# Kernel tuning notes

Hardware: AMD Instinct MI355X
Metric: run time of the kernel (lower is better)

## Reference

```python
import jax, jax.numpy as jnp
import numpy as np

B, SQ, C = 8, 4096, 1280
CAD = 2048
H, D = 20, 64          # heads x head_dim = hidden_size
NT = 4                 # num IP tokens
TXT = 77               # text tokens
IP_SCALE = 1.0


def setup_inputs() -> dict:
    key = jax.random.key(0)
    ks = jax.random.split(key, 9)
    s = 0.02
    return {
        "hidden_states": jax.random.normal(ks[0], (B, SQ, C), jnp.float32),
        "encoder_hidden_states": jax.random.normal(ks[1], (B, TXT + NT, CAD), jnp.float32),
        "Wq": jax.random.normal(ks[2], (C, C), jnp.float32) * s,
        "Wk": jax.random.normal(ks[3], (CAD, C), jnp.float32) * s,
        "Wv": jax.random.normal(ks[4], (CAD, C), jnp.float32) * s,
        "Wk_ip": jax.random.normal(ks[5], (CAD, C), jnp.float32) * s,
        "Wv_ip": jax.random.normal(ks[6], (CAD, C), jnp.float32) * s,
        "Wo": jax.random.normal(ks[7], (C, C), jnp.float32) * s,
        "bo": jnp.zeros((C,), jnp.float32),
    }


def _heads(x):
    # [b, s, C] -> [b, H, s, D]
    b, s, _ = x.shape
    return x.reshape(b, s, H, D).transpose(0, 2, 1, 3)


def _attend(q, k, v):
    scale = jnp.asarray(1.0 / np.sqrt(D), q.dtype)
    probs = jax.nn.softmax(jnp.einsum('bhqd,bhkd->bhqk', q, k) * scale, axis=-1)
    return jnp.einsum('bhqk,bhkd->bhqd', probs, v)


def reference(hidden_states, encoder_hidden_states, Wq, Wk, Wv, Wk_ip, Wv_ip, Wo, bo):
    residual = hidden_states
    txt = encoder_hidden_states[:, :-NT, :]   # [B, 77, CAD]
    ip = encoder_hidden_states[:, -NT:, :]    # [B, 4, CAD]

    q = _heads(hidden_states @ Wq)            # [B, H, SQ, D]
    k = _heads(txt @ Wk)
    v = _heads(txt @ Wv)
    out = _attend(q, k, v)                    # text branch

    ip_k = _heads(ip @ Wk_ip)
    ip_v = _heads(ip @ Wv_ip)
    out = out + IP_SCALE * _attend(q, ip_k, ip_v)  # IP-adapter branch

    b = out.shape[0]
    out = out.transpose(0, 2, 1, 3).reshape(b, SQ, C)  # merge heads
    out = out @ Wo + bo
    return out + residual
```

## Files before the change

kernel.cpp:

```cpp
#include <hip/hip_runtime.h>
#include <hip/hip_bf16.h>
#include <cstdint>
#include <cstddef>


typedef __bf16 bf16_t;
typedef __bf16 bf16x8 __attribute__((ext_vector_type(8)));
typedef __bf16 bf16x4 __attribute__((ext_vector_type(4)));
typedef float  f32x4  __attribute__((ext_vector_type(4)));
typedef unsigned int u32x4 __attribute__((ext_vector_type(4)));

using as3_void  = __attribute__((address_space(3))) void;
using as1_cvoid = const __attribute__((address_space(1))) void;

#define TXT_ 77

__device__ __forceinline__ bf16x8 ld16(const void* p) {
  u32x4 v = *(const u32x4*)p;
  return __builtin_bit_cast(bf16x8, v);
}

template <int EPI>
__global__ __launch_bounds__(512, 2)
void gemm256(const bf16_t* __restrict__ A, const bf16_t* __restrict__ Bt,
             void* __restrict__ Cout, int ntn, int N, int K,
             const float* __restrict__ bias, const void* __restrict__ residual)
{
  __shared__ __align__(16) char smem[131072];
  const int tid = threadIdx.x, lane = tid & 63, wid = tid >> 6;
  const int wm = wid >> 2, wn = wid & 3;

  const int nwg = gridDim.x;
  int g = blockIdx.x;
  if ((nwg & 7) == 0) g = (blockIdx.x & 7) * (nwg >> 3) + (blockIdx.x >> 3);
  const long bm = (long)(g / ntn) * 256;
  const long bn = (long)(g % ntn) * 256;

  const int NTk = K >> 5;

  const int srow = lane >> 2;
  const int scol = ((lane & 3) ^ ((lane >> 3) & 3)) * 8;

  auto stageA = [&](int t) {
    const int buf = t & 3;
    const long k0 = (long)t << 5;
#pragma unroll
    for (int j = 0; j < 2; ++j) {
      const int ci = j * 8 + wid;
      const bf16_t* gp = A + (bm + ci * 16 + srow) * (long)K + k0 + scol;
      __builtin_amdgcn_global_load_lds((as1_cvoid*)gp,
          (as3_void*)(smem + buf * 16384 + ci * 1024), 16, 0, 0);
    }
  };
  auto stageB = [&](int t) {
    const int buf = t & 3;
    const long k0 = (long)t << 5;
#pragma unroll
    for (int j = 0; j < 2; ++j) {
      const int ci = j * 8 + wid;
      const bf16_t* gp = Bt + (bn + ci * 16 + srow) * (long)K + k0 + scol;
      __builtin_amdgcn_global_load_lds((as1_cvoid*)gp,
          (as3_void*)(smem + 65536 + buf * 16384 + ci * 1024), 16, 0, 0);
    }
  };

  const int l15 = lane & 15, kq = lane >> 4;
  const int rc16 = (kq ^ ((l15 >> 1) & 3)) << 4;

  f32x4 acc[8][4] = {};

  stageA(0); stageB(0); stageA(1); stageB(1);
  asm volatile("s_waitcnt vmcnt(4)" ::: "memory");
  __builtin_amdgcn_s_barrier();

  for (int t = 0; t < NTk; ++t) {
    const char* sa = smem + (t & 3) * 16384;
    const char* sb = smem + 65536 + (t & 3) * 16384;
    bf16x8 bfr[4], afr[4];
#pragma unroll
    for (int n = 0; n < 4; ++n)
      bfr[n] = ld16(sb + (wn * 64 + n * 16 + l15) * 64 + rc16);
#pragma unroll
    for (int m = 0; m < 4; ++m)
      afr[m] = ld16(sa + (wm * 128 + m * 16 + l15) * 64 + rc16);
    if (t + 2 < NTk) stageA(t + 2);
    __builtin_amdgcn_s_setprio(1);
#pragma unroll
    for (int m = 0; m < 4; ++m)
#pragma unroll
      for (int n = 0; n < 4; ++n)
        acc[m][n] = __builtin_amdgcn_mfma_f32_16x16x32_bf16(afr[m], bfr[n], acc[m][n], 0, 0, 0);
    __builtin_amdgcn_s_setprio(0);
#pragma unroll
    for (int m = 0; m < 4; ++m)
      afr[m] = ld16(sa + (wm * 128 + (m + 4) * 16 + l15) * 64 + rc16);
    if (t + 2 < NTk) stageB(t + 2);
    __builtin_amdgcn_s_setprio(1);
#pragma unroll
    for (int m = 0; m < 4; ++m)
#pragma unroll
      for (int n = 0; n < 4; ++n)
        acc[m + 4][n] = __builtin_amdgcn_mfma_f32_16x16x32_bf16(afr[m], bfr[n], acc[m + 4][n], 0, 0, 0);
    __builtin_amdgcn_s_setprio(0);
    if (t == NTk - 2) asm volatile("s_waitcnt vmcnt(0)" ::: "memory");
    else              asm volatile("s_waitcnt vmcnt(4)" ::: "memory");
    __builtin_amdgcn_s_barrier();
    asm volatile("" ::: "memory");
  }

  const int orow0 = (lane >> 4) << 2;
#pragma unroll
  for (int m = 0; m < 8; ++m) {
#pragma unroll
    for (int n = 0; n < 4; ++n) {
      const long col = bn + wn * 64 + n * 16 + l15;
#pragma unroll
      for (int r = 0; r < 4; ++r) {
        const long row = bm + wm * 128 + m * 16 + orow0 + r;
        if constexpr (EPI == 0) {
          ((bf16_t*)Cout)[row * N + col] = (bf16_t)acc[m][n][r];
        } else {
          ((float*)Cout)[row * N + col] =
              acc[m][n][r] + bias[col] +
              (float)((const bf16_t*)residual)[row * N + col];
        }
      }
    }
  }
}

__global__ __launch_bounds__(256, 4)
void gemm_bt(const bf16_t* __restrict__ A, const bf16_t* __restrict__ Bt,
             bf16_t* __restrict__ Cout, int ntn, int N, int K)
{
  __shared__ __align__(16) char smem[2][16384];
  const int tid  = threadIdx.x;
  const int lane = tid & 63;
  const int wid  = tid >> 6;
  const int wm = wid >> 1, wn = wid & 1;

  const int g = blockIdx.x;
  const long bm = (long)(g / ntn) * 128;
  const long bn = (long)(g % ntn) * 128;

  f32x4 acc[4][4] = {};

  const int srow = lane >> 2;
  const int skb  = (lane & 3) ^ (((lane >> 2) ^ (lane >> 4)) & 3);
  const int NT = K >> 5;

  auto stage = [&](int buf, int kt) {
    const int k0 = kt << 5;
#pragma unroll
    for (int cc = 0; cc < 2; ++cc) {
      const int c = wid + cc * 4;
      const bf16_t* ga = A + (bm + c * 16 + srow) * (long)K + (k0 + skb * 8);
      __builtin_amdgcn_global_load_lds((as1_cvoid*)ga,
                                       (as3_void*)(&smem[buf][c * 1024]), 16, 0, 0);
      const bf16_t* gb = Bt + (bn + c * 16 + srow) * (long)K + (k0 + skb * 8);
      __builtin_amdgcn_global_load_lds((as1_cvoid*)gb,
                                       (as3_void*)(&smem[buf][8192 + c * 1024]), 16, 0, 0);
    }
  };

  const int rkb    = (((lane >> 4) ^ (lane & 3) ^ ((lane >> 2) & 3)) & 3) << 4;
  const int rrow_a = wm * 64 + (lane & 15);
  const int rrow_b = wn * 64 + (lane & 15);

  stage(0, 0);
  int cur = 0;
  for (int t = 0; t < NT; ++t) {
    __syncthreads();
    if (t + 1 < NT) stage(cur ^ 1, t + 1);
    const char* sa = smem[cur];
    const char* sb = smem[cur] + 8192;
    bf16x8 af[4], bfv[4];
#pragma unroll
    for (int m = 0; m < 4; ++m)
      af[m] = ld16(sa + (rrow_a + m * 16) * 64 + rkb);
#pragma unroll
    for (int n = 0; n < 4; ++n)
      bfv[n] = ld16(sb + (rrow_b + n * 16) * 64 + rkb);
#pragma unroll
    for (int m = 0; m < 4; ++m)
#pragma unroll
      for (int n = 0; n < 4; ++n)
        acc[m][n] = __builtin_amdgcn_mfma_f32_16x16x32_bf16(af[m], bfv[n], acc[m][n], 0, 0, 0);
    cur ^= 1;
  }

  const int orow0 = wm * 64 + ((lane >> 4) << 2);
  const int ocol0 = wn * 64 + (lane & 15);
#pragma unroll
  for (int m = 0; m < 4; ++m)
#pragma unroll
    for (int n = 0; n < 4; ++n) {
      const long col = bn + ocol0 + n * 16;
#pragma unroll
      for (int r = 0; r < 4; ++r)
        Cout[(bm + orow0 + m * 16 + r) * (long)N + col] = (bf16_t)acc[m][n][r];
    }
}

__global__ __launch_bounds__(256, 3)
void attn_fused(const bf16_t* __restrict__ q, const bf16_t* __restrict__ kvt,
                const bf16_t* __restrict__ kvip, bf16_t* __restrict__ outp)
{
  __shared__ __align__(16) bf16_t K_lds[80 * 64];
  __shared__ __align__(16) bf16_t Kip_lds[16 * 64];
  __shared__ __align__(16) bf16_t Vt_lds[64 * 128];
  __shared__ __align__(16) bf16_t P_lds[4][16 * 128];

  const int tid = threadIdx.x, lane = tid & 63, wid = tid >> 6;
  const int h = blockIdx.y, b = blockIdx.z;
  const int kvcol = h << 6;

  for (int idx = tid; idx < 640; idx += 256) {
    const int j = idx >> 3, c = idx & 7;
    bf16x8 v = {};
    if (j < TXT_) v = ld16(kvt + (long)(b * 80 + j) * 2560 + kvcol + c * 8);
    *(bf16x8*)((char*)K_lds + j * 128 + ((c ^ (j & 7)) << 4)) = v;
  }
  if (tid < 128) {
    const int j = tid >> 3, c = tid & 7;
    bf16x8 v = {};
    if (j < 4) v = ld16(kvip + (long)(b * 4 + j) * 2560 + kvcol + c * 8);
    *(bf16x8*)((char*)Kip_lds + j * 128 + ((c ^ (j & 7)) << 4)) = v;
  }
  for (int idx = tid; idx < 1024; idx += 256) {
    const int key = idx >> 3, c = idx & 7;
    bf16x8 v = {};
    if (key < TXT_)
      v = ld16(kvt + (long)(b * 80 + key) * 2560 + 1280 + kvcol + c * 8);
    else if (key >= 96 && key < 100)
      v = ld16(kvip + (long)(b * 4 + key - 96) * 2560 + 1280 + kvcol + c * 8);
#pragma unroll
    for (int e = 0; e < 8; ++e) {
      const int d = c * 8 + e;
      *(bf16_t*)((char*)Vt_lds + d * 256 + ((key * 2) ^ ((d & 7) << 4))) = v[e];
    }
  }
  for (int idx = tid; idx < 1024; idx += 256)
    *(bf16x8*)((char*)P_lds + idx * 16) = (bf16x8){};
  __syncthreads();

  const int l15 = lane & 15, hi = lane >> 4;
  const int dblk = hi << 3;
  const int prow0 = hi << 2;
  const float scale = 0.125f;
  char* const pw = (char*)P_lds[wid];

  const long qrow0 = (long)b * 4096 + ((long)blockIdx.x << 8) + (wid << 6);
  bf16x8 qf[4][2];
#pragma unroll
  for (int ms = 0; ms < 4; ++ms) {
    const bf16_t* qp = q + (qrow0 + ms * 16 + l15) * 1280 + kvcol;
    qf[ms][0] = ld16(qp + dblk);
    qf[ms][1] = ld16(qp + 32 + dblk);
  }

#pragma unroll
  for (int ms = 0; ms < 4; ++ms) {
    f32x4 sc[5];
#pragma unroll
    for (int t = 0; t < 5; ++t) {
      const int j = (t << 4) + l15;
      const bf16x8 k0 = ld16((char*)K_lds + j * 128 + ((hi ^ (j & 7)) << 4));
      const bf16x8 k1 = ld16((char*)K_lds + j * 128 + (((4 + hi) ^ (j & 7)) << 4));
      f32x4 z = {0.f, 0.f, 0.f, 0.f};
      z = __builtin_amdgcn_mfma_f32_16x16x32_bf16(qf[ms][0], k0, z, 0, 0, 0);
      z = __builtin_amdgcn_mfma_f32_16x16x32_bf16(qf[ms][1], k1, z, 0, 0, 0);
      sc[t] = z;
    }
#pragma unroll
    for (int t = 0; t < 5; ++t) {
      const bool valid = ((t << 4) + l15) < TXT_;
#pragma unroll
      for (int r = 0; r < 4; ++r)
        sc[t][r] = valid ? sc[t][r] * scale : -1e30f;
    }

#pragma unroll
    for (int r = 0; r < 4; ++r) {
      float m = sc[0][r];
#pragma unroll
      for (int t = 1; t < 5; ++t) m = fmaxf(m, sc[t][r]);
      m = fmaxf(m, __shfl_xor(m, 1));
      m = fmaxf(m, __shfl_xor(m, 2));
      m = fmaxf(m, __shfl_xor(m, 4));
      m = fmaxf(m, __shfl_xor(m, 8));
      float l = 0.f;
#pragma unroll
      for (int t = 0; t < 5; ++t) { const float p = __expf(sc[t][r] - m); sc[t][r] = p; l += p; }
      l += __shfl_xor(l, 1);
      l += __shfl_xor(l, 2);
      l += __shfl_xor(l, 4);
      l += __shfl_xor(l, 8);
      const float inv = 1.f / l;
      const int row = prow0 + r;
#pragma unroll
      for (int t = 0; t < 5; ++t)
        *(bf16_t*)(pw + row * 256 + ((((t << 4) + l15) * 2) ^ ((row & 7) << 4))) =
            (bf16_t)(sc[t][r] * inv);
    }

    {
      const bf16x8 ki0 = ld16((char*)Kip_lds + l15 * 128 + ((hi ^ (l15 & 7)) << 4));
      const bf16x8 ki1 = ld16((char*)Kip_lds + l15 * 128 + (((4 + hi) ^ (l15 & 7)) << 4));
      f32x4 z = {0.f, 0.f, 0.f, 0.f};
      z = __builtin_amdgcn_mfma_f32_16x16x32_bf16(qf[ms][0], ki0, z, 0, 0, 0);
      z = __builtin_amdgcn_mfma_f32_16x16x32_bf16(qf[ms][1], ki1, z, 0, 0, 0);
      const bool vip = l15 < 4;
#pragma unroll
      for (int r = 0; r < 4; ++r) {
        const float s = vip ? z[r] * scale : -1e30f;
        float m = s;
        m = fmaxf(m, __shfl_xor(m, 1));
        m = fmaxf(m, __shfl_xor(m, 2));
        m = fmaxf(m, __shfl_xor(m, 4));
        m = fmaxf(m, __shfl_xor(m, 8));
        const float p = __expf(s - m);
        float l = p;
        l += __shfl_xor(l, 1);
        l += __shfl_xor(l, 2);
        l += __shfl_xor(l, 4);
        l += __shfl_xor(l, 8);
        const int row = prow0 + r;
        *(bf16_t*)(pw + row * 256 + (((96 + l15) * 2) ^ ((row & 7) << 4))) =
            (bf16_t)(p * (1.f / l));
      }
    }

    f32x4 o[4] = {};
#pragma unroll
    for (int s = 0; s < 4; ++s) {
      const bf16x8 pa =
          ld16(pw + l15 * 256 + ((((s << 2) + hi) << 4) ^ ((l15 & 7) << 4)));
#pragma unroll
      for (int n = 0; n < 4; ++n) {
        const int d = (n << 4) + l15;
        const bf16x8 vb =
            ld16((char*)Vt_lds + d * 256 + ((((s << 2) + hi) << 4) ^ ((d & 7) << 4)));
        o[n] = __builtin_amdgcn_mfma_f32_16x16x32_bf16(pa, vb, o[n], 0, 0, 0);
      }
    }

    const long orow = qrow0 + ms * 16 + prow0;
#pragma unroll
    for (int n = 0; n < 4; ++n)
#pragma unroll
      for (int r = 0; r < 4; ++r)
        outp[(orow + r) * 1280 + kvcol + (n << 4) + l15] = (bf16_t)o[n][r];
  }
}

__global__ void cvt_bf16(const float* __restrict__ in, bf16_t* __restrict__ out, long n)
{
  const long i = ((long)blockIdx.x * 256 + threadIdx.x) * 4;
  if (i >= n) return;
  const float4 v = *(const float4*)(in + i);
  bf16x4 r;
  r[0] = (bf16_t)v.x; r[1] = (bf16_t)v.y; r[2] = (bf16_t)v.z; r[3] = (bf16_t)v.w;
  *(bf16x4*)(out + i) = r;
}

__global__ void transpose_cvt(const float* __restrict__ in, bf16_t* __restrict__ out,
                              int K, int N, int ostride)
{
  __shared__ float tile[32][33];
  const int k0 = blockIdx.x * 32, n0 = blockIdx.y * 32;
  for (int i = threadIdx.y; i < 32; i += 8)
    tile[i][threadIdx.x] = in[(long)(k0 + i) * N + n0 + threadIdx.x];
  __syncthreads();
  for (int i = threadIdx.y; i < 32; i += 8)
    out[(long)(n0 + i) * ostride + k0 + threadIdx.x] = (bf16_t)tile[threadIdx.x][i];
}

__global__ void pack_enc(const float* __restrict__ enc, bf16_t* __restrict__ a_txt,
                         bf16_t* __restrict__ a_ip)
{
  const long t4 = ((long)blockIdx.x * 256 + threadIdx.x) * 4;
  const long NTXT = 640L * 2048;
  bf16x4 r;
  r[0] = r[1] = r[2] = r[3] = (bf16_t)0.f;
  if (t4 < NTXT) {
    const int row = (int)(t4 >> 11), col = (int)(t4 & 2047);
    const int b = row / 80, j = row - b * 80;
    if (j < TXT_) {
      const float4 v = *(const float4*)(enc + (((long)(b * 81 + j)) << 11) + col);
      r[0] = (bf16_t)v.x; r[1] = (bf16_t)v.y; r[2] = (bf16_t)v.z; r[3] = (bf16_t)v.w;
    }
    *(bf16x4*)(a_txt + t4) = r;
  } else {
    const long u = t4 - NTXT;
    const int row = (int)(u >> 11), col = (int)(u & 2047);
    if (row < 32) {
      const int b = row >> 2, j = row & 3;
      const float4 v = *(const float4*)(enc + (((long)(b * 81 + TXT_ + j)) << 11) + col);
      r[0] = (bf16_t)v.x; r[1] = (bf16_t)v.y; r[2] = (bf16_t)v.z; r[3] = (bf16_t)v.w;
    }
    *(bf16x4*)(a_ip + u) = r;
  }
}

extern "C" void kernel_launch(void* const* d_in, const int* in_sizes, int n_in,
                              void* d_out, int out_size, void* d_ws, size_t ws_size,
                              hipStream_t stream)
{
  (void)in_sizes; (void)n_in; (void)out_size; (void)ws_size;
  const float* hs  = (const float*)d_in[0];
  const float* enc = (const float*)d_in[1];
  const float* Wq  = (const float*)d_in[2];
  const float* Wk  = (const float*)d_in[3];
  const float* Wv  = (const float*)d_in[4];
  const float* Wki = (const float*)d_in[5];
  const float* Wvi = (const float*)d_in[6];
  const float* Wo  = (const float*)d_in[7];
  const float* bo  = (const float*)d_in[8];

  char* ws = (char*)d_ws;
  size_t off = 0;
  auto alloc = [&](size_t bytes) {
    char* p = ws + off;
    off += (bytes + 255) & ~(size_t)255;
    return p;
  };
  bf16_t* buf1   = (bf16_t*)alloc(83886080);
  bf16_t* qb     = (bf16_t*)alloc(83886080);
  bf16_t* Wq_t   = (bf16_t*)alloc(3276800);
  bf16_t* Wo_t   = (bf16_t*)alloc(3276800);
  bf16_t* Wkv_t  = (bf16_t*)alloc(10485760);
  bf16_t* Wip_t  = (bf16_t*)alloc(10485760);
  bf16_t* a_txt  = (bf16_t*)alloc(2621440);
  bf16_t* a_ip   = (bf16_t*)alloc(524288);
  bf16_t* kv_txt = (bf16_t*)alloc(3276800);
  bf16_t* kv_ip  = (bf16_t*)alloc(655360);

  const dim3 tb(32, 8);
  cvt_bf16<<<40960, 256, 0, stream>>>(hs, buf1, 41943040L);
  transpose_cvt<<<dim3(40, 40), tb, 0, stream>>>(Wq, Wq_t, 1280, 1280, 1280);
  transpose_cvt<<<dim3(40, 40), tb, 0, stream>>>(Wo, Wo_t, 1280, 1280, 1280);
  transpose_cvt<<<dim3(64, 40), tb, 0, stream>>>(Wk, Wkv_t, 2048, 1280, 2048);
  transpose_cvt<<<dim3(64, 40), tb, 0, stream>>>(Wv, Wkv_t + (long)1280 * 2048, 2048, 1280, 2048);
  transpose_cvt<<<dim3(64, 40), tb, 0, stream>>>(Wki, Wip_t, 2048, 1280, 2048);
  transpose_cvt<<<dim3(64, 40), tb, 0, stream>>>(Wvi, Wip_t + (long)1280 * 2048, 2048, 1280, 2048);
  pack_enc<<<1536, 256, 0, stream>>>(enc, a_txt, a_ip);

  gemm256<0><<<640, 512, 0, stream>>>(buf1, Wq_t, qb, 5, 1280, 1280,
                                      nullptr, nullptr);
  gemm_bt<<<100, 256, 0, stream>>>(a_txt, Wkv_t, kv_txt, 20, 2560, 2048);
  gemm_bt<<<20, 256, 0, stream>>>(a_ip, Wip_t, kv_ip, 20, 2560, 2048);

  attn_fused<<<dim3(16, 20, 8), 256, 0, stream>>>(qb, kv_txt, kv_ip, qb);

  gemm256<2><<<640, 512, 0, stream>>>(qb, Wo_t, d_out, 5, 1280, 1280,
                                      bo, buf1);
}
```

Baseline: 484.8 us.

## Restructure GEMM mainloop to K=64 double-buffered tiles with quarter-staged prefetch

The 256x256 GEMM mainloop moves from a 4-deep ring of K=32 tiles to a 2-deep double buffer of K=64 tiles with a new 128-byte-row XOR swizzle. Each iteration splits into four MFMA phases, and each phase issues one quarter of the next tile's global-to-LDS loads. Every phase is bracketed by workgroup barriers and lgkmcnt waits. This aims to halve loop overhead and spread global loads across compute phases, but it adds more barriers and waits for all loads to finish at the end of every iteration (vmcnt(0)), which could expose memory latency.

```diff
diff --git a/kernel.cpp b/kernel.cpp
--- a/kernel.cpp
+++ b/kernel.cpp
@@ -35,55 +35,54 @@
   if ((nwg & 7) == 0) g = (blockIdx.x & 7) * (nwg >> 3) + (blockIdx.x >> 3);
   const long bm = (long)(g / ntn) * 256;
   const long bn = (long)(g % ntn) * 256;
-
-  const int NTk = K >> 5;
-
-  const int srow = lane >> 2;
-  const int scol = ((lane & 3) ^ ((lane >> 3) & 3)) * 8;
-
-  auto stageA = [&](int t) {
-    const int buf = t & 3;
-    const long k0 = (long)t << 5;
+  const int NTk = K >> 6;
+
+  const int srow = lane >> 3;
+  const int scol = ((lane & 7) ^ srow) * 8;
+
+  auto stage = [&](int mat, int h, int db, int u) {
+    const bf16_t* gbase = mat ? Bt : A;
+    const long rbase = (mat ? bn : bm) + h * 128 + wid * 8 + srow;
+    char* lbase = smem + mat * 65536 + db * 32768 + (h * 128 + wid * 8) * 128;
 #pragma unroll
     for (int j = 0; j < 2; ++j) {
-      const int ci = j * 8 + wid;
-      const bf16_t* gp = A + (bm + ci * 16 + srow) * (long)K + k0 + scol;
+      const bf16_t* gp = gbase + (rbase + j * 64) * (long)K + u * 64 + scol;
       __builtin_amdgcn_global_load_lds((as1_cvoid*)gp,
-          (as3_void*)(smem + buf * 16384 + ci * 1024), 16, 0, 0);
+                                       (as3_void*)(lbase + j * 8192), 16, 0, 0);
     }
   };
-  auto stageB = [&](int t) {
-    const int buf = t & 3;
-    const long k0 = (long)t << 5;
-#pragma unroll
-    for (int j = 0; j < 2; ++j) {
-      const int ci = j * 8 + wid;
-      const bf16_t* gp = Bt + (bn + ci * 16 + srow) * (long)K + k0 + scol;
-      __builtin_amdgcn_global_load_lds((as1_cvoid*)gp,
-          (as3_void*)(smem + 65536 + buf * 16384 + ci * 1024), 16, 0, 0);
-    }
+
+  const int l15 = lane & 15, kq = lane >> 4;
+  const int rswz = l15 & 7;
+
+  auto ldA = [&](int d, int m, int ks) {
+    return ld16(smem + d * 32768 + (wm * 128 + m * 16 + l15) * 128 +
+                (((ks * 4 + kq) ^ rswz) << 4));
   };
-
-  const int l15 = lane & 15, kq = lane >> 4;
-  const int rc16 = (kq ^ ((l15 >> 1) & 3)) << 4;
+  auto ldB = [&](int d, int n, int ks) {
+    return ld16(smem + 65536 + d * 32768 + (wn * 64 + n * 16 + l15) * 128 +
+                (((ks * 4 + kq) ^ rswz) << 4));
+  };
 
   f32x4 acc[8][4] = {};
-
-  stageA(0); stageB(0); stageA(1); stageB(1);
-  asm volatile("s_waitcnt vmcnt(4)" ::: "memory");
+  bf16x8 afr[4], bfr[4];
+
+  stage(0, 0, 0, 0); stage(0, 1, 0, 0); stage(1, 0, 0, 0); stage(1, 1, 0, 0);
+  asm volatile("s_waitcnt vmcnt(0)" ::: "memory");
   __builtin_amdgcn_s_barrier();
 
-  for (int t = 0; t < NTk; ++t) {
-    const char* sa = smem + (t & 3) * 16384;
-    const char* sb = smem + 65536 + (t & 3) * 16384;
-    bf16x8 bfr[4], afr[4];
-#pragma unroll
-    for (int n = 0; n < 4; ++n)
-      bfr[n] = ld16(sb + (wn * 64 + n * 16 + l15) * 64 + rc16);
-#pragma unroll
-    for (int m = 0; m < 4; ++m)
-      afr[m] = ld16(sa + (wm * 128 + m * 16 + l15) * 64 + rc16);
-    if (t + 2 < NTk) stageA(t + 2);
+  for (int u = 0; u < NTk; ++u) {
+    const int d = u & 1;
+    const bool pf = (u + 1 < NTk);
+
+#pragma unroll
+    for (int m = 0; m < 4; ++m) afr[m] = ldA(d, m, 0);
+#pragma unroll
+    for (int n = 0; n < 4; ++n) bfr[n] = ldB(d, n, 0);
+    if (pf) stage(0, 0, d ^ 1, u + 1);
+    __builtin_amdgcn_s_barrier();
+    asm volatile("s_waitcnt lgkmcnt(0)" ::: "memory");
+    __builtin_amdgcn_sched_barrier(0);
     __builtin_amdgcn_s_setprio(1);
 #pragma unroll
     for (int m = 0; m < 4; ++m)
@@ -91,10 +90,14 @@
       for (int n = 0; n < 4; ++n)
         acc[m][n] = __builtin_amdgcn_mfma_f32_16x16x32_bf16(afr[m], bfr[n], acc[m][n], 0, 0, 0);
     __builtin_amdgcn_s_setprio(0);
-#pragma unroll
-    for (int m = 0; m < 4; ++m)
-      afr[m] = ld16(sa + (wm * 128 + (m + 4) * 16 + l15) * 64 + rc16);
-    if (t + 2 < NTk) stageB(t + 2);
+    __builtin_amdgcn_s_barrier();
+
+#pragma unroll
+    for (int m = 0; m < 4; ++m) afr[m] = ldA(d, m + 4, 0);
+    if (pf) stage(0, 1, d ^ 1, u + 1);
+    __builtin_amdgcn_s_barrier();
+    asm volatile("s_waitcnt lgkmcnt(0)" ::: "memory");
+    __builtin_amdgcn_sched_barrier(0);
     __builtin_amdgcn_s_setprio(1);
 #pragma unroll
     for (int m = 0; m < 4; ++m)
@@ -102,10 +105,40 @@
       for (int n = 0; n < 4; ++n)
         acc[m + 4][n] = __builtin_amdgcn_mfma_f32_16x16x32_bf16(afr[m], bfr[n], acc[m + 4][n], 0, 0, 0);
     __builtin_amdgcn_s_setprio(0);
-    if (t == NTk - 2) asm volatile("s_waitcnt vmcnt(0)" ::: "memory");
-    else              asm volatile("s_waitcnt vmcnt(4)" ::: "memory");
-    __builtin_amdgcn_s_barrier();
-    asm volatile("" ::: "memory");
+    __builtin_amdgcn_s_barrier();
+
+#pragma unroll
+    for (int m = 0; m < 4; ++m) afr[m] = ldA(d, m, 1);
+#pragma unroll
+    for (int n = 0; n < 4; ++n) bfr[n] = ldB(d, n, 1);
+    if (pf) stage(1, 0, d ^ 1, u + 1);
+    __builtin_amdgcn_s_barrier();
+    asm volatile("s_waitcnt lgkmcnt(0)" ::: "memory");
+    __builtin_amdgcn_sched_barrier(0);
+    __builtin_amdgcn_s_setprio(1);
+#pragma unroll
+    for (int m = 0; m < 4; ++m)
+#pragma unroll
+      for (int n = 0; n < 4; ++n)
+        acc[m][n] = __builtin_amdgcn_mfma_f32_16x16x32_bf16(afr[m], bfr[n], acc[m][n], 0, 0, 0);
+    __builtin_amdgcn_s_setprio(0);
+    __builtin_amdgcn_s_barrier();
+
+#pragma unroll
+    for (int m = 0; m < 4; ++m) afr[m] = ldA(d, m + 4, 1);
+    if (pf) stage(1, 1, d ^ 1, u + 1);
+    __builtin_amdgcn_s_barrier();
+    asm volatile("s_waitcnt lgkmcnt(0)" ::: "memory");
+    __builtin_amdgcn_sched_barrier(0);
+    __builtin_amdgcn_s_setprio(1);
+#pragma unroll
+    for (int m = 0; m < 4; ++m)
+#pragma unroll
+      for (int n = 0; n < 4; ++n)
+        acc[m + 4][n] = __builtin_amdgcn_mfma_f32_16x16x32_bf16(afr[m], bfr[n], acc[m + 4][n], 0, 0, 0);
+    __builtin_amdgcn_s_setprio(0);
+    asm volatile("s_waitcnt vmcnt(0)" ::: "memory");
+    __builtin_amdgcn_s_barrier();
   }
 
   const int orow0 = (lane >> 4) << 2;
```

After: 496.2 us. +2.3%, slower.
